# Kernel tuning notes

Measured on AMD Instinct MI355X. Metric: run time of the kernel, lower is better.

The kernel has to match this reference:

```python
import jax, jax.numpy as jnp
import numpy as np

C = 256       # in_channels
IC = 128      # inter_channels = C // 2
G = 4         # num_group
D = IC // G   # per-group channels = 32
B, H, W_ = 4, 56, 56
EPS = 1e-5


def conv1x1(x, w, b=None):
    # x: (B,Cin,H,W), w: (Cout,Cin)
    y = jnp.einsum('bchw,oc->bohw', x, w)
    if b is not None:
        y = y + b[None, :, None, None]
    return y


def bn(x, scale, bias, mean, var):
    inv = scale / jnp.sqrt(var + EPS)
    return x * inv[None, :, None, None] + (bias - mean * inv)[None, :, None, None]


def setup_inputs():
    key = jax.random.key(0)
    ks = jax.random.split(key, 16)
    r = lambda k, shape, s=0.05: jax.random.normal(k, shape, jnp.float32) * s
    C4 = C // 4
    return {
        'x': jax.random.normal(ks[0], (B, C, H, W_), jnp.float32),
        'g_w': r(ks[1], (IC, C)), 'g_b': r(ks[2], (IC,)),
        'theta_w': r(ks[3], (IC, C)), 'theta_b': r(ks[4], (IC,)),
        'phi_w': r(ks[5], (IC, C)), 'phi_b': r(ks[6], (IC,)),
        'W_w': r(ks[7], (C, IC)), 'W_b': r(ks[8], (C,)),
        'bnW_scale': jnp.ones((C,)), 'bnW_bias': jnp.zeros((C,)),
        'bnW_mean': jnp.zeros((C,)), 'bnW_var': jnp.ones((C,)),
        'ff1_w': r(ks[9], (C4, C)),
        'ffbn1_scale': jnp.ones((C4,)), 'ffbn1_bias': jnp.zeros((C4,)),
        'ffbn1_mean': jnp.zeros((C4,)), 'ffbn1_var': jnp.ones((C4,)),
        'ff2_w': r(ks[10], (C4, C4, 3, 3)),
        'ffbn2_scale': jnp.ones((C4,)), 'ffbn2_bias': jnp.zeros((C4,)),
        'ffbn2_mean': jnp.zeros((C4,)), 'ffbn2_var': jnp.ones((C4,)),
        'ff3_w': r(ks[11], (C, C4)),
        'ffbn3_scale': jnp.ones((C,)), 'ffbn3_bias': jnp.zeros((C,)),
        'ffbn3_mean': jnp.zeros((C,)), 'ffbn3_var': jnp.ones((C,)),
    }


def reference(x, g_w, g_b, theta_w, theta_b, phi_w, phi_b, W_w, W_b,
              bnW_scale, bnW_bias, bnW_mean, bnW_var,
              ff1_w, ffbn1_scale, ffbn1_bias, ffbn1_mean, ffbn1_var,
              ff2_w, ffbn2_scale, ffbn2_bias, ffbn2_mean, ffbn2_var,
              ff3_w, ffbn3_scale, ffbn3_bias, ffbn3_mean, ffbn3_var):
    b, c, h, w = x.shape
    n = h * w
    # grouped non-local attention: channels split into G groups of D
    gx = conv1x1(x, g_w, g_b).reshape(b, G, D, n)       # (B,G,D,N)
    tx = conv1x1(x, theta_w, theta_b).reshape(b, G, D, n)
    px = conv1x1(x, phi_w, phi_b).reshape(b, G, D, n)
    f = jnp.einsum('bgdn,bgdm->bgnm', tx, px)           # (B,G,N,N) scores
    attn = jax.nn.softmax(f, axis=-1)                   # softmax over keys (torch dim=2 on (b,N,N))
    yy = jnp.einsum('bgnm,bgdm->bgdn', attn, gx)        # (B,G,D,N)
    y_out = yy.reshape(b, IC, h, w)
    W_y = bn(conv1x1(y_out, W_w, W_b), bnW_scale, bnW_bias, bnW_mean, bnW_var)
    z = jax.nn.relu(W_y + x)
    # FPNFFConv bottleneck FFN (BN in eval mode)
    o = jax.nn.relu(bn(conv1x1(z, ff1_w), ffbn1_scale, ffbn1_bias, ffbn1_mean, ffbn1_var))
    o = jax.lax.conv_general_dilated(o, ff2_w, (1, 1), 'SAME',
                                     dimension_numbers=('NCHW', 'OIHW', 'NCHW'))
    o = jax.nn.relu(bn(o, ffbn2_scale, ffbn2_bias, ffbn2_mean, ffbn2_var))
    o = bn(conv1x1(o, ff3_w), ffbn3_scale, ffbn3_bias, ffbn3_mean, ffbn3_var)
    return jax.nn.relu(o + z)
```

## Files before the change

### kernel.cpp

```cpp
#include <hip/hip_runtime.h>
#include <hip/hip_bf16.h>

#define NPIX 3136
#define BB 4

typedef unsigned short u16;
typedef __bf16 bf16x8 __attribute__((ext_vector_type(8)));
typedef float f32x4 __attribute__((ext_vector_type(4)));

__device__ __forceinline__ float b2f(u16 u) {
  union { unsigned u; float f; } c; c.u = ((unsigned)u) << 16; return c.f;
}
__device__ __forceinline__ u16 f2b(float f) {
  __hip_bfloat16 h = __float2bfloat16(f);
  return *reinterpret_cast<u16*>(&h);
}
__device__ __forceinline__ unsigned pk2(float a, float b) {
  return (unsigned)f2b(a) | ((unsigned)f2b(b) << 16);
}

template<int NSTEP>
__device__ __forceinline__ void mf_gemm(const u16* __restrict__ Arow, int strideA,
                                        const u16* __restrict__ Brow, int strideB,
                                        int lq, f32x4 acc[4]) {
#pragma unroll
  for (int s = 0; s < NSTEP; ++s) {
    bf16x8 af = *(const bf16x8*)(Arow + s * 32 + lq * 8);
#pragma unroll
    for (int ot = 0; ot < 4; ++ot) {
      bf16x8 bf = *(const bf16x8*)(Brow + (size_t)ot * 16 * strideB + s * 32 + lq * 8);
      acc[ot] = __builtin_amdgcn_mfma_f32_16x16x32_bf16(af, bf, acc[ot], 0, 0, 0);
    }
  }
}

__global__ __launch_bounds__(256) void prep_w(
    const float* __restrict__ gw, const float* __restrict__ tw,
    const float* __restrict__ pw, const float* __restrict__ Ww,
    const float* __restrict__ f1w, const float* __restrict__ f2w,
    const float* __restrict__ f3w,
    u16* __restrict__ gwb, u16* __restrict__ twb, u16* __restrict__ pwb,
    u16* __restrict__ Wwb, u16* __restrict__ f1b, u16* __restrict__ f3b,
    u16* __restrict__ f2p) {
  for (int i = blockIdx.x * 256 + threadIdx.x; i < 200704; i += gridDim.x * 256) {
    int j = i;
    if (j < 32768) { gwb[j] = f2b(gw[j]); continue; } j -= 32768;
    if (j < 32768) { twb[j] = f2b(tw[j]); continue; } j -= 32768;
    if (j < 32768) { pwb[j] = f2b(pw[j]); continue; } j -= 32768;
    if (j < 32768) { Wwb[j] = f2b(Ww[j]); continue; } j -= 32768;
    if (j < 16384) { f1b[j] = f2b(f1w[j]); continue; } j -= 16384;
    if (j < 16384) { f3b[j] = f2b(f3w[j]); continue; } j -= 16384;
    int t = j >> 12, rem = j & 4095, co = rem >> 6, ci = rem & 63;
    f2p[j] = f2b(f2w[(co * 64 + ci) * 9 + t]);
  }
}

__global__ __launch_bounds__(256) void prep_x(const float* __restrict__ x,
                                              u16* __restrict__ xt) {
  __shared__ u16 sT[64 * 65];
  const int b = blockIdx.z, c0 = blockIdx.y * 64, n0 = blockIdx.x * 64;
  const int t = threadIdx.x;
#pragma unroll
  for (int cc = 0; cc < 4; ++cc) {
    int c = cc * 16 + (t >> 4), n4 = (t & 15) * 4;
    float4 v = *(const float4*)(x + ((size_t)(b * 256 + c0 + c)) * NPIX + n0 + n4);
    sT[c * 65 + n4 + 0] = f2b(v.x);
    sT[c * 65 + n4 + 1] = f2b(v.y);
    sT[c * 65 + n4 + 2] = f2b(v.z);
    sT[c * 65 + n4 + 3] = f2b(v.w);
  }
  __syncthreads();
#pragma unroll
  for (int nn = 0; nn < 4; ++nn) {
    int n = nn * 16 + (t >> 4), c4 = (t & 15) * 4;
    uint2 s;
    s.x = (unsigned)sT[(c4 + 0) * 65 + n] | ((unsigned)sT[(c4 + 1) * 65 + n] << 16);
    s.y = (unsigned)sT[(c4 + 2) * 65 + n] | ((unsigned)sT[(c4 + 3) * 65 + n] << 16);
    *(uint2*)(xt + ((size_t)b * NPIX + n0 + n) * 256 + c0 + c4) = s;
  }
}

__global__ __launch_bounds__(256) void proj_kernel(
    const u16* __restrict__ xt,
    const u16* __restrict__ gwb, const u16* __restrict__ twb, const u16* __restrict__ pwb,
    const float* __restrict__ gb, const float* __restrict__ tb, const float* __restrict__ pb,
    u16* __restrict__ gx, u16* __restrict__ Tq, u16* __restrict__ Pk) {
  const int b = blockIdx.z, oc = blockIdx.y, nb = blockIdx.x * 64;
  const int sec = oc >> 1, rbase = (oc & 1) * 64;
  const u16* wsel = sec == 0 ? gwb : (sec == 1 ? twb : pwb);
  const float* bsel = sec == 0 ? gb : (sec == 1 ? tb : pb);
  const int wv = threadIdx.x >> 6, lane = threadIdx.x & 63;
  const int lr = lane & 15, lq = lane >> 4;
  const int nrow = nb + wv * 16;
  f32x4 acc[4] = {};
  mf_gemm<8>(xt + ((size_t)b * NPIX + nrow + lr) * 256, 256,
             wsel + (size_t)(rbase + lr) * 256, 256, lq, acc);
#pragma unroll
  for (int ot = 0; ot < 4; ++ot) {
    const int o = rbase + ot * 16 + lr;
    const float bias = bsel[o];
    if (sec == 0) {
#pragma unroll
      for (int r = 0; r < 4; ++r)
        gx[((size_t)b * 128 + o) * NPIX + nrow + lq * 4 + r] = f2b(acc[ot][r] + bias);
    } else {
      const int g = o >> 5, dl = o & 31;
      u16* dst = sec == 1 ? Tq : Pk;
      size_t base = (size_t)(b * 4 + g) * NPIX;
#pragma unroll
      for (int r = 0; r < 4; ++r)
        dst[(base + nrow + lq * 4 + r) * 32 + dl] = f2b(acc[ot][r] + bias);
    }
  }
}

__global__ __launch_bounds__(256) void attn_kernel(
    const u16* __restrict__ Tq, const u16* __restrict__ Pk,
    const u16* __restrict__ gx, float* __restrict__ OP, float* __restrict__ LP) {
  __shared__ __align__(16) u16 Plds[4][32][40];
  const int bid = blockIdx.x;
  const int ks = bid / 400, rem = bid % 400;
  const int bg = rem / 25, qblk = rem % 25;
  const int b = bg >> 2, g = bg & 3;
  const int wave = threadIdx.x >> 6, lane = threadIdx.x & 63;
  const int lr = lane & 15, lq = lane >> 4;
  const int qbase = qblk * 128 + wave * 32;
  const int kc0 = ks * 800;
  const int kc1 = (kc0 + 800 < NPIX) ? kc0 + 800 : NPIX;
  const u16* Qp = Tq + (size_t)bg * NPIX * 32;
  const u16* Kp = Pk + (size_t)bg * NPIX * 32;
  const u16* Vp = gx + ((size_t)b * 128 + g * 32) * NPIX;

  bf16x8 qf[2];
#pragma unroll
  for (int qi = 0; qi < 2; ++qi) {
    int row = qbase + qi * 16 + lr;
    row = row < NPIX ? row : NPIX - 1;
    qf[qi] = *(const bf16x8*)(Qp + (size_t)row * 32 + lq * 8);
  }
  const f32x4 z4 = {0.f, 0.f, 0.f, 0.f};
  f32x4 O[2][2], Lf[2];
#pragma unroll
  for (int qi = 0; qi < 2; ++qi) { O[qi][0] = z4; O[qi][1] = z4; Lf[qi] = z4; }
  bf16x8 onef;
#pragma unroll
  for (int j = 0; j < 8; ++j) onef[j] = (__bf16)1.0f;

  for (int kc = kc0; kc < kc1; kc += 32) {
    bf16x8 kf0 = *(const bf16x8*)(Kp + (size_t)(kc + lr) * 32 + lq * 8);
    bf16x8 kf1 = *(const bf16x8*)(Kp + (size_t)(kc + 16 + lr) * 32 + lq * 8);
    f32x4 S[2][2];
    S[0][0] = __builtin_amdgcn_mfma_f32_16x16x32_bf16(qf[0], kf0, z4, 0, 0, 0);
    S[0][1] = __builtin_amdgcn_mfma_f32_16x16x32_bf16(qf[0], kf1, z4, 0, 0, 0);
    S[1][0] = __builtin_amdgcn_mfma_f32_16x16x32_bf16(qf[1], kf0, z4, 0, 0, 0);
    S[1][1] = __builtin_amdgcn_mfma_f32_16x16x32_bf16(qf[1], kf1, z4, 0, 0, 0);
#pragma unroll
    for (int qi = 0; qi < 2; ++qi)
#pragma unroll
      for (int kt = 0; kt < 2; ++kt)
#pragma unroll
        for (int r = 0; r < 4; ++r) {
          float p = __expf(fminf(S[qi][kt][r], 60.f));
          Plds[wave][qi * 16 + lq * 4 + r][kt * 16 + lr] = f2b(p);
        }
    bf16x8 pf0 = *(const bf16x8*)(&Plds[wave][lr][lq * 8]);
    bf16x8 pf1 = *(const bf16x8*)(&Plds[wave][16 + lr][lq * 8]);
    bf16x8 vf0 = *(const bf16x8*)(Vp + (size_t)lr * NPIX + kc + lq * 8);
    bf16x8 vf1 = *(const bf16x8*)(Vp + (size_t)(16 + lr) * NPIX + kc + lq * 8);
    O[0][0] = __builtin_amdgcn_mfma_f32_16x16x32_bf16(pf0, vf0, O[0][0], 0, 0, 0);
    O[0][1] = __builtin_amdgcn_mfma_f32_16x16x32_bf16(pf0, vf1, O[0][1], 0, 0, 0);
    O[1][0] = __builtin_amdgcn_mfma_f32_16x16x32_bf16(pf1, vf0, O[1][0], 0, 0, 0);
    O[1][1] = __builtin_amdgcn_mfma_f32_16x16x32_bf16(pf1, vf1, O[1][1], 0, 0, 0);
    Lf[0] = __builtin_amdgcn_mfma_f32_16x16x32_bf16(pf0, onef, Lf[0], 0, 0, 0);
    Lf[1] = __builtin_amdgcn_mfma_f32_16x16x32_bf16(pf1, onef, Lf[1], 0, 0, 0);
  }
  const size_t sbase = (size_t)(ks * 16 + bg) * NPIX;
#pragma unroll
  for (int qi = 0; qi < 2; ++qi) {
#pragma unroll
    for (int r = 0; r < 4; ++r) {
      int qrow = qbase + qi * 16 + lq * 4 + r;
      if (qrow < NPIX) {
        size_t ob = (sbase + qrow) * 32;
        OP[ob + lr] = O[qi][0][r];
        OP[ob + 16 + lr] = O[qi][1][r];
        if (lr == 0) LP[sbase + qrow] = Lf[qi][r];
      }
    }
  }
}

__global__ __launch_bounds__(256) void combine_kernel(
    const float* __restrict__ OP, const float* __restrict__ LP,
    u16* __restrict__ yt) {
  const int bg = blockIdx.y, b = bg >> 2, g = bg & 3;
  const int t = threadIdx.x;
  const int n = blockIdx.x * 64 + (t >> 2);
  const int dseg = (t & 3) * 8;
  float4 a0 = {0, 0, 0, 0}, a1 = {0, 0, 0, 0};
  float l = 0.f;
#pragma unroll
  for (int ks = 0; ks < 4; ++ks) {
    size_t base = ((size_t)(ks * 16 + bg) * NPIX + n) * 32 + dseg;
    float4 v0 = *(const float4*)(OP + base);
    float4 v1 = *(const float4*)(OP + base + 4);
    a0.x += v0.x; a0.y += v0.y; a0.z += v0.z; a0.w += v0.w;
    a1.x += v1.x; a1.y += v1.y; a1.z += v1.z; a1.w += v1.w;
    l += LP[(size_t)(ks * 16 + bg) * NPIX + n];
  }
  float inv = 1.0f / l;
  uint4 s;
  s.x = pk2(a0.x * inv, a0.y * inv);
  s.y = pk2(a0.z * inv, a0.w * inv);
  s.z = pk2(a1.x * inv, a1.y * inv);
  s.w = pk2(a1.z * inv, a1.w * inv);
  *(uint4*)(yt + ((size_t)b * NPIX + n) * 128 + g * 32 + dseg) = s;
}

__global__ __launch_bounds__(256) void wz_kernel(
    const u16* __restrict__ yt, const u16* __restrict__ Wwb, const float* __restrict__ Wb,
    const float* __restrict__ sc, const float* __restrict__ bi,
    const float* __restrict__ mu, const float* __restrict__ var,
    const float* __restrict__ x, u16* __restrict__ zt) {
  const int b = blockIdx.z, oc = blockIdx.y, nb = blockIdx.x * 64;
  const int wv = threadIdx.x >> 6, lane = threadIdx.x & 63;
  const int lr = lane & 15, lq = lane >> 4;
  const int nrow = nb + wv * 16;
  f32x4 acc[4] = {};
  mf_gemm<4>(yt + ((size_t)b * NPIX + nrow + lr) * 128, 128,
             Wwb + (size_t)(oc * 64 + lr) * 128, 128, lq, acc);
#pragma unroll
  for (int ot = 0; ot < 4; ++ot) {
    const int o = oc * 64 + ot * 16 + lr;
    float inv = sc[o] * rsqrtf(var[o] + 1e-5f);
    float off = bi[o] - mu[o] * inv + Wb[o] * inv;
    float4 xr = *(const float4*)(x + ((size_t)b * 256 + o) * NPIX + nrow + lq * 4);
    float xv[4] = {xr.x, xr.y, xr.z, xr.w};
#pragma unroll
    for (int r = 0; r < 4; ++r) {
      float v = fmaxf(acc[ot][r] * inv + off + xv[r], 0.f);
      zt[((size_t)b * NPIX + nrow + lq * 4 + r) * 256 + o] = f2b(v);
    }
  }
}

__global__ __launch_bounds__(256) void ff1_kernel(
    const u16* __restrict__ zt, const u16* __restrict__ f1b,
    const float* __restrict__ sc, const float* __restrict__ bi,
    const float* __restrict__ mu, const float* __restrict__ var,
    u16* __restrict__ o1t) {
  const int b = blockIdx.z, nb = blockIdx.x * 64;
  const int wv = threadIdx.x >> 6, lane = threadIdx.x & 63;
  const int lr = lane & 15, lq = lane >> 4;
  const int nrow = nb + wv * 16;
  f32x4 acc[4] = {};
  mf_gemm<8>(zt + ((size_t)b * NPIX + nrow + lr) * 256, 256,
             f1b + (size_t)lr * 256, 256, lq, acc);
#pragma unroll
  for (int ot = 0; ot < 4; ++ot) {
    const int o = ot * 16 + lr;
    float inv = sc[o] * rsqrtf(var[o] + 1e-5f);
    float off = bi[o] - mu[o] * inv;
#pragma unroll
    for (int r = 0; r < 4; ++r) {
      float v = fmaxf(acc[ot][r] * inv + off, 0.f);
      o1t[((size_t)b * NPIX + nrow + lq * 4 + r) * 64 + o] = f2b(v);
    }
  }
}

__global__ __launch_bounds__(256) void ff2_kernel(
    const u16* __restrict__ o1t, const u16* __restrict__ f2p,
    const float* __restrict__ sc, const float* __restrict__ bi,
    const float* __restrict__ mu, const float* __restrict__ var,
    u16* __restrict__ o2t) {
  const int b = blockIdx.z, nb = blockIdx.x * 64;
  const int wv = threadIdx.x >> 6, lane = threadIdx.x & 63;
  const int lr = lane & 15, lq = lane >> 4;
  const int n_row = nb + wv * 16 + lr;
  const int h = n_row / 56, w = n_row % 56;
  f32x4 acc[4] = {};
#pragma unroll
  for (int t = 0; t < 9; ++t) {
    const int dh = t / 3 - 1, dw = t % 3 - 1;
    const bool valid = (h + dh) >= 0 && (h + dh) < 56 && (w + dw) >= 0 && (w + dw) < 56;
    const u16* Ar = o1t + ((size_t)b * NPIX + n_row + dh * 56 + dw) * 64;
    const u16* Br = f2p + ((size_t)t * 64 + lr) * 64;
#pragma unroll
    for (int k2 = 0; k2 < 2; ++k2) {
      bf16x8 af = {};
      if (valid) af = *(const bf16x8*)(Ar + k2 * 32 + lq * 8);
#pragma unroll
      for (int ot = 0; ot < 4; ++ot) {
        bf16x8 bf = *(const bf16x8*)(Br + (size_t)ot * 16 * 64 + k2 * 32 + lq * 8);
        acc[ot] = __builtin_amdgcn_mfma_f32_16x16x32_bf16(af, bf, acc[ot], 0, 0, 0);
      }
    }
  }
  const int nrow = nb + wv * 16;
#pragma unroll
  for (int ot = 0; ot < 4; ++ot) {
    const int o = ot * 16 + lr;
    float inv = sc[o] * rsqrtf(var[o] + 1e-5f);
    float off = bi[o] - mu[o] * inv;
#pragma unroll
    for (int r = 0; r < 4; ++r) {
      float v = fmaxf(acc[ot][r] * inv + off, 0.f);
      o2t[((size_t)b * NPIX + nrow + lq * 4 + r) * 64 + o] = f2b(v);
    }
  }
}

__global__ __launch_bounds__(256) void ff3_kernel(
    const u16* __restrict__ o2t, const u16* __restrict__ f3b,
    const float* __restrict__ sc, const float* __restrict__ bi,
    const float* __restrict__ mu, const float* __restrict__ var,
    const u16* __restrict__ zt, float* __restrict__ out) {
  const int b = blockIdx.z, oc = blockIdx.y, nb = blockIdx.x * 64;
  const int wv = threadIdx.x >> 6, lane = threadIdx.x & 63;
  const int lr = lane & 15, lq = lane >> 4;
  const int nrow = nb + wv * 16;
  f32x4 acc[4] = {};
  mf_gemm<2>(o2t + ((size_t)b * NPIX + nrow + lr) * 64, 64,
             f3b + (size_t)(oc * 64 + lr) * 64, 64, lq, acc);
#pragma unroll
  for (int ot = 0; ot < 4; ++ot) {
    const int o = oc * 64 + ot * 16 + lr;
    float inv = sc[o] * rsqrtf(var[o] + 1e-5f);
    float off = bi[o] - mu[o] * inv;
    float4 s;
    float* sv = (float*)&s;
#pragma unroll
    for (int r = 0; r < 4; ++r) {
      float zres = b2f(zt[((size_t)b * NPIX + nrow + lq * 4 + r) * 256 + o]);
      sv[r] = fmaxf(acc[ot][r] * inv + off + zres, 0.f);
    }
    *(float4*)(out + ((size_t)b * 256 + o) * NPIX + nrow + lq * 4) = s;
  }
}

extern "C" void kernel_launch(void* const* d_in, const int* in_sizes, int n_in,
                              void* d_out, int out_size, void* d_ws, size_t ws_size,
                              hipStream_t stream) {
  const float* x    = (const float*)d_in[0];
  const float* gw   = (const float*)d_in[1];
  const float* gb   = (const float*)d_in[2];
  const float* tw   = (const float*)d_in[3];
  const float* tb   = (const float*)d_in[4];
  const float* pw   = (const float*)d_in[5];
  const float* pb   = (const float*)d_in[6];
  const float* Ww   = (const float*)d_in[7];
  const float* Wb   = (const float*)d_in[8];
  const float* bnWs = (const float*)d_in[9];
  const float* bnWb = (const float*)d_in[10];
  const float* bnWm = (const float*)d_in[11];
  const float* bnWv = (const float*)d_in[12];
  const float* f1w  = (const float*)d_in[13];
  const float* b1s  = (const float*)d_in[14];
  const float* b1b  = (const float*)d_in[15];
  const float* b1m  = (const float*)d_in[16];
  const float* b1v  = (const float*)d_in[17];
  const float* f2w  = (const float*)d_in[18];
  const float* b2s  = (const float*)d_in[19];
  const float* b2b  = (const float*)d_in[20];
  const float* b2m  = (const float*)d_in[21];
  const float* b2v  = (const float*)d_in[22];
  const float* f3w  = (const float*)d_in[23];
  const float* b3s  = (const float*)d_in[24];
  const float* b3b  = (const float*)d_in[25];
  const float* b3m  = (const float*)d_in[26];
  const float* b3v  = (const float*)d_in[27];
  float* out = (float*)d_out;

  u16* p = (u16*)d_ws;
  u16* xt  = p; p += (size_t)BB * NPIX * 256;
  u16* gwb = p; p += 128 * 256;
  u16* twb = p; p += 128 * 256;
  u16* pwb = p; p += 128 * 256;
  u16* Wwb = p; p += 256 * 128;
  u16* f1b = p; p += 64 * 256;
  u16* f3b = p; p += 256 * 64;
  u16* f2p = p; p += 9 * 64 * 64;
  u16* Tq  = p; p += (size_t)16 * NPIX * 32;
  u16* Pk  = p; p += (size_t)16 * NPIX * 32;
  u16* gx  = p; p += (size_t)BB * 128 * NPIX;
  u16* yt  = p; p += (size_t)BB * NPIX * 128;
  float* OP = (float*)p;
  float* LP = OP + (size_t)4 * 16 * NPIX * 32;
  u16* zt  = (u16*)OP;
  u16* o1t = zt + (size_t)BB * NPIX * 256;
  u16* o2t = o1t + (size_t)BB * NPIX * 64;

  prep_w<<<dim3(196), 256, 0, stream>>>(gw, tw, pw, Ww, f1w, f2w, f3w,
                                        gwb, twb, pwb, Wwb, f1b, f3b, f2p);
  prep_x<<<dim3(49, 4, BB), 256, 0, stream>>>(x, xt);
  proj_kernel<<<dim3(49, 6, BB), 256, 0, stream>>>(xt, gwb, twb, pwb, gb, tb, pb,
                                                   gx, Tq, Pk);
  attn_kernel<<<dim3(1600), 256, 0, stream>>>(Tq, Pk, gx, OP, LP);
  combine_kernel<<<dim3(49, 16), 256, 0, stream>>>(OP, LP, yt);
  wz_kernel<<<dim3(49, 4, BB), 256, 0, stream>>>(yt, Wwb, Wb, bnWs, bnWb, bnWm, bnWv,
                                                 x, zt);
  ff1_kernel<<<dim3(49, 1, BB), 256, 0, stream>>>(zt, f1b, b1s, b1b, b1m, b1v, o1t);
  ff2_kernel<<<dim3(49, 1, BB), 256, 0, stream>>>(o1t, f2p, b2s, b2b, b2m, b2v, o2t);
  ff3_kernel<<<dim3(49, 4, BB), 256, 0, stream>>>(o2t, f3b, b3s, b3b, b3m, b3v, zt, out);
}
```

Baseline: 262.3 us.

## Fold log2e into theta, prefetch K/V in attention, bf16 partials, split FFN channels

Folds log2(e) into the theta weights and bias so the attention kernel can use exp2 directly without clamping, and truncates P to bf16 by bit shift. The attention kernel now uses one 16-row query tile per wave with a doubled grid and software-prefetches the next K/V fragments. Partial outputs are stored as bf16 to cut combine traffic, and the ff1/ff2 kernels split output channels across two blocks for more parallelism. Removing the clamp risks overflow for large scores, and bf16 partials and truncation lose some precision.

```diff
diff --git a/kernel.cpp b/kernel.cpp
--- a/kernel.cpp
+++ b/kernel.cpp
@@ -3,6 +3,7 @@
 
 #define NPIX 3136
 #define BB 4
+#define LOG2E 1.4426950408889634f
 
 typedef unsigned short u16;
 typedef __bf16 bf16x8 __attribute__((ext_vector_type(8)));
@@ -19,16 +20,16 @@
   return (unsigned)f2b(a) | ((unsigned)f2b(b) << 16);
 }
 
-template<int NSTEP>
-__device__ __forceinline__ void mf_gemm(const u16* __restrict__ Arow, int strideA,
-                                        const u16* __restrict__ Brow, int strideB,
-                                        int lq, f32x4 acc[4]) {
+template<int NSTEP, int NOT>
+__device__ __forceinline__ void mf_gemm(const u16* __restrict__ Arow, int sA,
+                                        const u16* __restrict__ Brow, int sB,
+                                        int lq, f32x4* acc) {
 #pragma unroll
   for (int s = 0; s < NSTEP; ++s) {
     bf16x8 af = *(const bf16x8*)(Arow + s * 32 + lq * 8);
 #pragma unroll
-    for (int ot = 0; ot < 4; ++ot) {
-      bf16x8 bf = *(const bf16x8*)(Brow + (size_t)ot * 16 * strideB + s * 32 + lq * 8);
+    for (int ot = 0; ot < NOT; ++ot) {
+      bf16x8 bf = *(const bf16x8*)(Brow + (size_t)ot * 16 * sB + s * 32 + lq * 8);
       acc[ot] = __builtin_amdgcn_mfma_f32_16x16x32_bf16(af, bf, acc[ot], 0, 0, 0);
     }
   }
@@ -45,7 +46,7 @@
   for (int i = blockIdx.x * 256 + threadIdx.x; i < 200704; i += gridDim.x * 256) {
     int j = i;
     if (j < 32768) { gwb[j] = f2b(gw[j]); continue; } j -= 32768;
-    if (j < 32768) { twb[j] = f2b(tw[j]); continue; } j -= 32768;
+    if (j < 32768) { twb[j] = f2b(tw[j] * LOG2E); continue; } j -= 32768;
     if (j < 32768) { pwb[j] = f2b(pw[j]); continue; } j -= 32768;
     if (j < 32768) { Wwb[j] = f2b(Ww[j]); continue; } j -= 32768;
     if (j < 16384) { f1b[j] = f2b(f1w[j]); continue; } j -= 16384;
@@ -93,12 +94,13 @@
   const int lr = lane & 15, lq = lane >> 4;
   const int nrow = nb + wv * 16;
   f32x4 acc[4] = {};
-  mf_gemm<8>(xt + ((size_t)b * NPIX + nrow + lr) * 256, 256,
-             wsel + (size_t)(rbase + lr) * 256, 256, lq, acc);
+  mf_gemm<8, 4>(xt + ((size_t)b * NPIX + nrow + lr) * 256, 256,
+                wsel + (size_t)(rbase + lr) * 256, 256, lq, acc);
 #pragma unroll
   for (int ot = 0; ot < 4; ++ot) {
     const int o = rbase + ot * 16 + lr;
-    const float bias = bsel[o];
+    float bias = bsel[o];
+    if (sec == 1) bias *= LOG2E;
     if (sec == 0) {
 #pragma unroll
       for (int r = 0; r < 4; ++r)
@@ -116,104 +118,94 @@
 
 __global__ __launch_bounds__(256) void attn_kernel(
     const u16* __restrict__ Tq, const u16* __restrict__ Pk,
-    const u16* __restrict__ gx, float* __restrict__ OP, float* __restrict__ LP) {
-  __shared__ __align__(16) u16 Plds[4][32][40];
+    const u16* __restrict__ gx, u16* __restrict__ OPb, float* __restrict__ LP) {
+  __shared__ __align__(16) u16 Plds[4][16][40];
   const int bid = blockIdx.x;
-  const int ks = bid / 400, rem = bid % 400;
-  const int bg = rem / 25, qblk = rem % 25;
+  const int qblk = bid % 49, rem = bid / 49;
+  const int bg = rem & 15, ks = rem >> 4;
   const int b = bg >> 2, g = bg & 3;
   const int wave = threadIdx.x >> 6, lane = threadIdx.x & 63;
   const int lr = lane & 15, lq = lane >> 4;
-  const int qbase = qblk * 128 + wave * 32;
+  const int qbase = qblk * 64 + wave * 16;
   const int kc0 = ks * 800;
   const int kc1 = (kc0 + 800 < NPIX) ? kc0 + 800 : NPIX;
   const u16* Qp = Tq + (size_t)bg * NPIX * 32;
   const u16* Kp = Pk + (size_t)bg * NPIX * 32;
   const u16* Vp = gx + ((size_t)b * 128 + g * 32) * NPIX;
 
-  bf16x8 qf[2];
-#pragma unroll
-  for (int qi = 0; qi < 2; ++qi) {
-    int row = qbase + qi * 16 + lr;
-    row = row < NPIX ? row : NPIX - 1;
-    qf[qi] = *(const bf16x8*)(Qp + (size_t)row * 32 + lq * 8);
-  }
+  bf16x8 qf = *(const bf16x8*)(Qp + (size_t)(qbase + lr) * 32 + lq * 8);
   const f32x4 z4 = {0.f, 0.f, 0.f, 0.f};
-  f32x4 O[2][2], Lf[2];
-#pragma unroll
-  for (int qi = 0; qi < 2; ++qi) { O[qi][0] = z4; O[qi][1] = z4; Lf[qi] = z4; }
+  f32x4 O0 = z4, O1 = z4, L4 = z4;
   bf16x8 onef;
 #pragma unroll
   for (int j = 0; j < 8; ++j) onef[j] = (__bf16)1.0f;
 
+  bf16x8 kf0 = *(const bf16x8*)(Kp + (size_t)(kc0 + lr) * 32 + lq * 8);
+  bf16x8 kf1 = *(const bf16x8*)(Kp + (size_t)(kc0 + 16 + lr) * 32 + lq * 8);
+  bf16x8 vf0 = *(const bf16x8*)(Vp + (size_t)lr * NPIX + kc0 + lq * 8);
+  bf16x8 vf1 = *(const bf16x8*)(Vp + (size_t)(16 + lr) * NPIX + kc0 + lq * 8);
+
   for (int kc = kc0; kc < kc1; kc += 32) {
-    bf16x8 kf0 = *(const bf16x8*)(Kp + (size_t)(kc + lr) * 32 + lq * 8);
-    bf16x8 kf1 = *(const bf16x8*)(Kp + (size_t)(kc + 16 + lr) * 32 + lq * 8);
-    f32x4 S[2][2];
-    S[0][0] = __builtin_amdgcn_mfma_f32_16x16x32_bf16(qf[0], kf0, z4, 0, 0, 0);
-    S[0][1] = __builtin_amdgcn_mfma_f32_16x16x32_bf16(qf[0], kf1, z4, 0, 0, 0);
-    S[1][0] = __builtin_amdgcn_mfma_f32_16x16x32_bf16(qf[1], kf0, z4, 0, 0, 0);
-    S[1][1] = __builtin_amdgcn_mfma_f32_16x16x32_bf16(qf[1], kf1, z4, 0, 0, 0);
-#pragma unroll
-    for (int qi = 0; qi < 2; ++qi)
-#pragma unroll
-      for (int kt = 0; kt < 2; ++kt)
-#pragma unroll
-        for (int r = 0; r < 4; ++r) {
-          float p = __expf(fminf(S[qi][kt][r], 60.f));
-          Plds[wave][qi * 16 + lq * 4 + r][kt * 16 + lr] = f2b(p);
-        }
-    bf16x8 pf0 = *(const bf16x8*)(&Plds[wave][lr][lq * 8]);
-    bf16x8 pf1 = *(const bf16x8*)(&Plds[wave][16 + lr][lq * 8]);
-    bf16x8 vf0 = *(const bf16x8*)(Vp + (size_t)lr * NPIX + kc + lq * 8);
-    bf16x8 vf1 = *(const bf16x8*)(Vp + (size_t)(16 + lr) * NPIX + kc + lq * 8);
-    O[0][0] = __builtin_amdgcn_mfma_f32_16x16x32_bf16(pf0, vf0, O[0][0], 0, 0, 0);
-    O[0][1] = __builtin_amdgcn_mfma_f32_16x16x32_bf16(pf0, vf1, O[0][1], 0, 0, 0);
-    O[1][0] = __builtin_amdgcn_mfma_f32_16x16x32_bf16(pf1, vf0, O[1][0], 0, 0, 0);
-    O[1][1] = __builtin_amdgcn_mfma_f32_16x16x32_bf16(pf1, vf1, O[1][1], 0, 0, 0);
-    Lf[0] = __builtin_amdgcn_mfma_f32_16x16x32_bf16(pf0, onef, Lf[0], 0, 0, 0);
-    Lf[1] = __builtin_amdgcn_mfma_f32_16x16x32_bf16(pf1, onef, Lf[1], 0, 0, 0);
+    int nkc = kc + 32;
+    if (nkc >= kc1) nkc = kc0;
+    bf16x8 nk0 = *(const bf16x8*)(Kp + (size_t)(nkc + lr) * 32 + lq * 8);
+    bf16x8 nk1 = *(const bf16x8*)(Kp + (size_t)(nkc + 16 + lr) * 32 + lq * 8);
+    bf16x8 nv0 = *(const bf16x8*)(Vp + (size_t)lr * NPIX + nkc + lq * 8);
+    bf16x8 nv1 = *(const bf16x8*)(Vp + (size_t)(16 + lr) * NPIX + nkc + lq * 8);
+
+    f32x4 S0 = __builtin_amdgcn_mfma_f32_16x16x32_bf16(qf, kf0, z4, 0, 0, 0);
+    f32x4 S1 = __builtin_amdgcn_mfma_f32_16x16x32_bf16(qf, kf1, z4, 0, 0, 0);
+#pragma unroll
+    for (int r = 0; r < 4; ++r) {
+      unsigned u0 = __builtin_bit_cast(unsigned, __builtin_exp2f(S0[r]));
+      unsigned u1 = __builtin_bit_cast(unsigned, __builtin_exp2f(S1[r]));
+      Plds[wave][lq * 4 + r][lr] = (u16)(u0 >> 16);
+      Plds[wave][lq * 4 + r][16 + lr] = (u16)(u1 >> 16);
+    }
+    bf16x8 pf = *(const bf16x8*)(&Plds[wave][lr][lq * 8]);
+    O0 = __builtin_amdgcn_mfma_f32_16x16x32_bf16(pf, vf0, O0, 0, 0, 0);
+    O1 = __builtin_amdgcn_mfma_f32_16x16x32_bf16(pf, vf1, O1, 0, 0, 0);
+    L4 = __builtin_amdgcn_mfma_f32_16x16x32_bf16(pf, onef, L4, 0, 0, 0);
+    kf0 = nk0; kf1 = nk1; vf0 = nv0; vf1 = nv1;
   }
   const size_t sbase = (size_t)(ks * 16 + bg) * NPIX;
-#pragma unroll
-  for (int qi = 0; qi < 2; ++qi) {
-#pragma unroll
-    for (int r = 0; r < 4; ++r) {
-      int qrow = qbase + qi * 16 + lq * 4 + r;
-      if (qrow < NPIX) {
-        size_t ob = (sbase + qrow) * 32;
-        OP[ob + lr] = O[qi][0][r];
-        OP[ob + 16 + lr] = O[qi][1][r];
-        if (lr == 0) LP[sbase + qrow] = Lf[qi][r];
-      }
-    }
+  const int q0 = qbase + lq * 4;
+#pragma unroll
+  for (int r = 0; r < 4; ++r) {
+    size_t ob = (sbase + q0 + r) * 32;
+    OPb[ob + lr] = f2b(O0[r]);
+    OPb[ob + 16 + lr] = f2b(O1[r]);
+    if (lr == 0) LP[sbase + q0 + r] = L4[r];
   }
 }
 
 __global__ __launch_bounds__(256) void combine_kernel(
-    const float* __restrict__ OP, const float* __restrict__ LP,
+    const u16* __restrict__ OPb, const float* __restrict__ LP,
     u16* __restrict__ yt) {
   const int bg = blockIdx.y, b = bg >> 2, g = bg & 3;
   const int t = threadIdx.x;
   const int n = blockIdx.x * 64 + (t >> 2);
   const int dseg = (t & 3) * 8;
-  float4 a0 = {0, 0, 0, 0}, a1 = {0, 0, 0, 0};
+  float a[8] = {};
   float l = 0.f;
 #pragma unroll
   for (int ks = 0; ks < 4; ++ks) {
-    size_t base = ((size_t)(ks * 16 + bg) * NPIX + n) * 32 + dseg;
-    float4 v0 = *(const float4*)(OP + base);
-    float4 v1 = *(const float4*)(OP + base + 4);
-    a0.x += v0.x; a0.y += v0.y; a0.z += v0.z; a0.w += v0.w;
-    a1.x += v1.x; a1.y += v1.y; a1.z += v1.z; a1.w += v1.w;
+    const u16* src = OPb + ((size_t)(ks * 16 + bg) * NPIX + n) * 32 + dseg;
+    uint4 v = *(const uint4*)src;
+    const unsigned* vp = (const unsigned*)&v;
+#pragma unroll
+    for (int k = 0; k < 4; ++k) {
+      a[2 * k] += b2f((u16)vp[k]);
+      a[2 * k + 1] += b2f((u16)(vp[k] >> 16));
+    }
     l += LP[(size_t)(ks * 16 + bg) * NPIX + n];
   }
   float inv = 1.0f / l;
   uint4 s;
-  s.x = pk2(a0.x * inv, a0.y * inv);
-  s.y = pk2(a0.z * inv, a0.w * inv);
-  s.z = pk2(a1.x * inv, a1.y * inv);
-  s.w = pk2(a1.z * inv, a1.w * inv);
+  s.x = pk2(a[0] * inv, a[1] * inv);
+  s.y = pk2(a[2] * inv, a[3] * inv);
+  s.z = pk2(a[4] * inv, a[5] * inv);
+  s.w = pk2(a[6] * inv, a[7] * inv);
   *(uint4*)(yt + ((size_t)b * NPIX + n) * 128 + g * 32 + dseg) = s;
 }
 
@@ -227,8 +219,8 @@
   const int lr = lane & 15, lq = lane >> 4;
   const int nrow = nb + wv * 16;
   f32x4 acc[4] = {};
-  mf_gemm<4>(yt + ((size_t)b * NPIX + nrow + lr) * 128, 128,
-             Wwb + (size_t)(oc * 64 + lr) * 128, 128, lq, acc);
+  mf_gemm<4, 4>(yt + ((size_t)b * NPIX + nrow + lr) * 128, 128,
+                Wwb + (size_t)(oc * 64 + lr) * 128, 128, lq, acc);
 #pragma unroll
   for (int ot = 0; ot < 4; ++ot) {
     const int o = oc * 64 + ot * 16 + lr;
@@ -249,16 +241,16 @@
     const float* __restrict__ sc, const float* __restrict__ bi,
     const float* __restrict__ mu, const float* __restrict__ var,
     u16* __restrict__ o1t) {
-  const int b = blockIdx.z, nb = blockIdx.x * 64;
-  const int wv = threadIdx.x >> 6, lane = threadIdx.x & 63;
-  const int lr = lane & 15, lq = lane >> 4;
-  const int nrow = nb + wv * 16;
-  f32x4 acc[4] = {};
-  mf_gemm<8>(zt + ((size_t)b * NPIX + nrow + lr) * 256, 256,
-             f1b + (size_t)lr * 256, 256, lq, acc);
-#pragma unroll
-  for (int ot = 0; ot < 4; ++ot) {
-    const int o = ot * 16 + lr;
+  const int b = blockIdx.z, oc = blockIdx.y, nb = blockIdx.x * 64;
+  const int wv = threadIdx.x >> 6, lane = threadIdx.x & 63;
+  const int lr = lane & 15, lq = lane >> 4;
+  const int nrow = nb + wv * 16;
+  f32x4 acc[2] = {};
+  mf_gemm<8, 2>(zt + ((size_t)b * NPIX + nrow + lr) * 256, 256,
+                f1b + (size_t)(oc * 32 + lr) * 256, 256, lq, acc);
+#pragma unroll
+  for (int ot = 0; ot < 2; ++ot) {
+    const int o = oc * 32 + ot * 16 + lr;
     float inv = sc[o] * rsqrtf(var[o] + 1e-5f);
     float off = bi[o] - mu[o] * inv;
 #pragma unroll
@@ -274,24 +266,24 @@
     const float* __restrict__ sc, const float* __restrict__ bi,
     const float* __restrict__ mu, const float* __restrict__ var,
     u16* __restrict__ o2t) {
-  const int b = blockIdx.z, nb = blockIdx.x * 64;
+  const int b = blockIdx.z, oc = blockIdx.y, nb = blockIdx.x * 64;
   const int wv = threadIdx.x >> 6, lane = threadIdx.x & 63;
   const int lr = lane & 15, lq = lane >> 4;
   const int n_row = nb + wv * 16 + lr;
   const int h = n_row / 56, w = n_row % 56;
-  f32x4 acc[4] = {};
+  f32x4 acc[2] = {};
 #pragma unroll
   for (int t = 0; t < 9; ++t) {
     const int dh = t / 3 - 1, dw = t % 3 - 1;
     const bool valid = (h + dh) >= 0 && (h + dh) < 56 && (w + dw) >= 0 && (w + dw) < 56;
     const u16* Ar = o1t + ((size_t)b * NPIX + n_row + dh * 56 + dw) * 64;
-    const u16* Br = f2p + ((size_t)t * 64 + lr) * 64;
+    const u16* Br = f2p + (size_t)t * 4096 + (size_t)(oc * 32 + lr) * 64;
 #pragma unroll
     for (int k2 = 0; k2 < 2; ++k2) {
       bf16x8 af = {};
       if (valid) af = *(const bf16x8*)(Ar + k2 * 32 + lq * 8);
 #pragma unroll
-      for (int ot = 0; ot < 4; ++ot) {
+      for (int ot = 0; ot < 2; ++ot) {
         bf16x8 bf = *(const bf16x8*)(Br + (size_t)ot * 16 * 64 + k2 * 32 + lq * 8);
         acc[ot] = __builtin_amdgcn_mfma_f32_16x16x32_bf16(af, bf, acc[ot], 0, 0, 0);
       }
@@ -299,8 +291,8 @@
   }
   const int nrow = nb + wv * 16;
 #pragma unroll
-  for (int ot = 0; ot < 4; ++ot) {
-    const int o = ot * 16 + lr;
+  for (int ot = 0; ot < 2; ++ot) {
+    const int o = oc * 32 + ot * 16 + lr;
     float inv = sc[o] * rsqrtf(var[o] + 1e-5f);
     float off = bi[o] - mu[o] * inv;
 #pragma unroll
@@ -321,8 +313,8 @@
   const int lr = lane & 15, lq = lane >> 4;
   const int nrow = nb + wv * 16;
   f32x4 acc[4] = {};
-  mf_gemm<2>(o2t + ((size_t)b * NPIX + nrow + lr) * 64, 64,
-             f3b + (size_t)(oc * 64 + lr) * 64, 64, lq, acc);
+  mf_gemm<2, 4>(o2t + ((size_t)b * NPIX + nrow + lr) * 64, 64,
+                f3b + (size_t)(oc * 64 + lr) * 64, 64, lq, acc);
 #pragma unroll
   for (int ot = 0; ot < 4; ++ot) {
     const int o = oc * 64 + ot * 16 + lr;
@@ -385,22 +377,22 @@
   u16* Pk  = p; p += (size_t)16 * NPIX * 32;
   u16* gx  = p; p += (size_t)BB * 128 * NPIX;
   u16* yt  = p; p += (size_t)BB * NPIX * 128;
-  float* OP = (float*)p;
-  float* LP = OP + (size_t)4 * 16 * NPIX * 32;
-  u16* zt  = (u16*)OP;
-  u16* o1t = zt + (size_t)BB * NPIX * 256;
-  u16* o2t = o1t + (size_t)BB * NPIX * 64;
+  u16* OPb = p; p += (size_t)4 * 16 * NPIX * 32;
+  float* LP = (float*)p; p += (size_t)4 * 16 * NPIX * 2;
+  u16* zt  = p; p += (size_t)BB * NPIX * 256;
+  u16* o1t = p; p += (size_t)BB * NPIX * 64;
+  u16* o2t = p; p += (size_t)BB * NPIX * 64;
 
   prep_w<<<dim3(196), 256, 0, stream>>>(gw, tw, pw, Ww, f1w, f2w, f3w,
                                         gwb, twb, pwb, Wwb, f1b, f3b, f2p);
   prep_x<<<dim3(49, 4, BB), 256, 0, stream>>>(x, xt);
   proj_kernel<<<dim3(49, 6, BB), 256, 0, stream>>>(xt, gwb, twb, pwb, gb, tb, pb,
                                                    gx, Tq, Pk);
-  attn_kernel<<<dim3(1600), 256, 0, stream>>>(Tq, Pk, gx, OP, LP);
-  combine_kernel<<<dim3(49, 16), 256, 0, stream>>>(OP, LP, yt);
+  attn_kernel<<<dim3(3136), 256, 0, stream>>>(Tq, Pk, gx, OPb, LP);
+  combine_kernel<<<dim3(49, 16), 256, 0, stream>>>(OPb, LP, yt);
   wz_kernel<<<dim3(49, 4, BB), 256, 0, stream>>>(yt, Wwb, Wb, bnWs, bnWb, bnWm, bnWv,
                                                  x, zt);
-  ff1_kernel<<<dim3(49, 1, BB), 256, 0, stream>>>(zt, f1b, b1s, b1b, b1m, b1v, o1t);
-  ff2_kernel<<<dim3(49, 1, BB), 256, 0, stream>>>(o1t, f2p, b2s, b2b, b2m, b2v, o2t);
+  ff1_kernel<<<dim3(49, 2, BB), 256, 0, stream>>>(zt, f1b, b1s, b1b, b1m, b1v, o1t);
+  ff2_kernel<<<dim3(49, 2, BB), 256, 0, stream>>>(o1t, f2p, b2s, b2b, b2m, b2v, o2t);
   ff3_kernel<<<dim3(49, 4, BB), 256, 0, stream>>>(o2t, f3b, b3s, b3b, b3m, b3v, zt, out);
 }
```

Result: slower. 314.0 us (+19.7%).
